# Performance work log

Hardware: AMD Instinct MI355X
Metric: run time of the kernel (lower is better)

Reference implementation:

```python
import jax, jax.numpy as jnp
import numpy as np

B, MAX_LEN, V, H, E = 256, 31, 10000, 512, 512


def setup_inputs() -> dict:
    key = jax.random.key(0)
    ks = jax.random.split(key, 10)
    s = 0.05
    return {
        "global_images": jax.random.normal(ks[0], (B, E), jnp.float32),
        "w_input": jax.random.randint(ks[1], (B, MAX_LEN), 0, V),
        "caption_lengths": jax.random.randint(ks[2], (B,), 2, MAX_LEN + 1),
        "emb": jax.random.normal(ks[3], (V, E), jnp.float32) * s,
        "W_ih": jax.random.normal(ks[4], (4 * H, 2 * E), jnp.float32) * s,
        "W_hh": jax.random.normal(ks[5], (4 * H, H), jnp.float32) * s,
        "b_ih": jax.random.normal(ks[6], (4 * H,), jnp.float32) * s,
        "b_hh": jax.random.normal(ks[7], (4 * H,), jnp.float32) * s,
        "W_out": jax.random.normal(ks[8], (V, H), jnp.float32) * s,
        "b_out": jax.random.normal(ks[9], (V,), jnp.float32) * s,
    }


def reference(global_images, w_input, caption_lengths, emb, W_ih, W_hh, b_ih, b_hh, W_out, b_out):
    # Sort by caption length, descending (mirrors torch .sort(descending=True))
    order = jnp.argsort(-caption_lengths)
    lens = caption_lengths[order]
    w = w_input[order]                      # [B, max_len]
    g = global_images[order]                # [B, E]
    target = w[:, 1:]                       # [B, max_len-1]
    dec_len = lens - 1                      # has_end_seq_token=True

    T = w.shape[1] - 1                      # max decode steps
    h0 = jnp.zeros((g.shape[0], W_hh.shape[1]), dtype=g.dtype)
    c0 = jnp.zeros_like(h0)
    words = w[:, :T].T                      # [T, B]
    ts = jnp.arange(T)

    def step(carry, inp):
        h, c = carry
        w_t, t = inp
        x_t = jnp.concatenate([g, emb[w_t]], axis=1)          # [B, 2E]
        gates = x_t @ W_ih.T + b_ih + h @ W_hh.T + b_hh       # [B, 4H]
        i, f, gg, o = jnp.split(gates, 4, axis=1)
        i, f, o = jax.nn.sigmoid(i), jax.nn.sigmoid(f), jax.nn.sigmoid(o)
        gg = jnp.tanh(gg)
        c_new = f * c + i * gg
        h_new = o * jnp.tanh(c_new)
        active = (t < dec_len)[:, None]                       # shrinking active batch
        h = jnp.where(active, h_new, h)
        c = jnp.where(active, c_new, c)
        pt = jax.nn.log_softmax(h_new @ W_out.T + b_out, axis=1)
        pt = jnp.where(active, pt, jnp.zeros((), pt.dtype))
        return (h, c), pt

    (_, _), preds = jax.lax.scan(step, (h0, c0), (words, ts))
    preds = jnp.transpose(preds, (1, 0, 2))                   # [B, T, V]
    preds = jnp.pad(preds, ((0, 0), (0, 1), (0, 0)))          # -> [B, max_len, V]
    return preds, target, dec_len
```

## Files before the change

### kernel.cpp

```cpp
#include <hip/hip_runtime.h>
#include <hip/hip_bf16.h>
#include <math.h>

#define NB   256
#define ML   31
#define NT   30
#define NV   10000
#define NH   512
#define NE   512
#define NG   2048

#define OFF_TGT  (256LL*31LL*10000LL)
#define OFF_DEC  (OFF_TGT + 256LL*30LL)
#define PRED_B   (31LL*10000LL)

typedef __attribute__((ext_vector_type(8))) short bf16x8;
typedef __attribute__((ext_vector_type(4))) float f32x4;

__device__ inline unsigned short f2bf(float f) {
    unsigned int x = __float_as_uint(f);
    unsigned int r = x + 0x7FFFu + ((x >> 16) & 1u);
    return (unsigned short)(r >> 16);
}
__device__ inline float bf2f(unsigned short u) {
    return __uint_as_float((unsigned int)u << 16);
}

__device__ inline void gl2lds16(const void* g, void* l) {
    __builtin_amdgcn_global_load_lds(
        (const __attribute__((address_space(1))) unsigned int*)g,
        (__attribute__((address_space(3))) unsigned int*)l, 16, 0, 0);
}

__global__ void sort_k(const int* __restrict__ lens, int* __restrict__ order,
                       int* __restrict__ cnt, int* __restrict__ start,
                       float* __restrict__ out_dec) {
    __shared__ int sd[NB];
    int i = threadIdx.x;
    int li = lens[i];
    int r = 0;
    for (int j = 0; j < NB; j++) {
        int lj = lens[j];
        r += (lj > li) || (lj == li && j < i);
    }
    order[r] = i;
    out_dec[r] = (float)(li - 1);
    sd[r] = li - 1;
    __syncthreads();
    if (i < NT) {
        int c = 0;
        for (int b = 0; b < NB; b++) c += (sd[b] > i);
        cnt[i] = c;
    }
    __syncthreads();
    if (i == 0) {
        int s = 0;
        for (int t = 0; t < NT; t++) { start[t] = s; s += cnt[t]; }
        start[NT] = s;
    }
}

__global__ void gather_k(const float* __restrict__ gimg, const int* __restrict__ w_in,
                         const int* __restrict__ order,
                         unsigned short* __restrict__ g_sb, int* __restrict__ wsort,
                         float* __restrict__ out_tgt) {
    int r = blockIdx.x, tid = threadIdx.x;
    int o = order[r];
    for (int e = tid; e < NE; e += 256)
        g_sb[r * NE + e] = f2bf(gimg[o * NE + e]);
    if (tid < ML) wsort[r * ML + tid] = w_in[o * ML + tid];
    if (tid < NT) out_tgt[r * NT + tid] = (float)w_in[o * ML + tid + 1];
}

__global__ void rowlist_k(const int* __restrict__ wsort, const int* __restrict__ cnt,
                          const int* __restrict__ start,
                          int* __restrict__ rowlist, int* __restrict__ rowwc) {
    int t = blockIdx.x, b = threadIdx.x;
    if (b < cnt[t]) {
        int pos = start[t] + b;
        rowlist[pos] = t * 256 + b;
        rowwc[pos] = wsort[b * ML + t];
    }
}

__global__ void f2b_k(const float* __restrict__ src, unsigned short* __restrict__ dst, int n4) {
    int i = blockIdx.x * 256 + threadIdx.x;
    if (i >= n4) return;
    float4 v = ((const float4*)src)[i];
    ushort4 o;
    o.x = f2bf(v.x); o.y = f2bf(v.y); o.z = f2bf(v.z); o.w = f2bf(v.w);
    ((ushort4*)dst)[i] = o;
}

__global__ void wih_k(const float* __restrict__ W_ih, unsigned short* __restrict__ dst, int koff) {
    int gid = blockIdx.x * 256 + threadIdx.x;
    int j = gid >> 7, k4 = gid & 127;
    float4 v = *(const float4*)(W_ih + (size_t)j * (2 * NE) + koff + k4 * 4);
    ushort4 o;
    o.x = f2bf(v.x); o.y = f2bf(v.y); o.z = f2bf(v.z); o.w = f2bf(v.w);
    *(ushort4*)(dst + (size_t)j * NE + k4 * 4) = o;
}

__global__ void wimg2_k(const float* __restrict__ W_hh, unsigned short* __restrict__ Wimg2) {
    int gid = blockIdx.x * 256 + threadIdx.x;
    int hi = gid & 3, kt = (gid >> 2) & 15, R = (gid >> 6) & 127, s = gid >> 13;
    int q = R >> 5, ct = (R >> 4) & 1, lo = R & 15;
    int col = q * 512 + s * 32 + ct * 16 + lo;
    int k = kt * 32 + hi * 8;
    const float* src = W_hh + (size_t)col * NH + k;
    __align__(16) unsigned short o[8];
#pragma unroll
    for (int j = 0; j < 8; ++j) o[j] = f2bf(src[j]);
    int ba = (R << 10) + ((kt * 64 + hi * 16) ^ ((lo & 7) << 4));
    *(uint4*)((char*)Wimg2 + ((size_t)s << 17) + ba) = *(const uint4*)o;
}

__global__ void pad_k(float* __restrict__ out) {
    int gid = blockIdx.x * 256 + threadIdx.x;
    if (gid < NB * NV) {
        int b = gid / NV, v = gid % NV;
        out[(size_t)b * PRED_B + (size_t)NT * NV + v] = 0.f;
    }
}
__global__ void zero_k(float* __restrict__ p, int n) {
    int i = blockIdx.x * 256 + threadIdx.x;
    if (i < n) p[i] = 0.f;
}

template <int AMODE, int EPI>
__launch_bounds__(256)
__global__ void bgemm(const unsigned short* __restrict__ Abf,
                      const int* __restrict__ ridx,
                      const unsigned short* __restrict__ Aemb,
                      const unsigned short* __restrict__ Bbf,
                      int N,
                      const int* __restrict__ mact_p,
                      const float* __restrict__ bias1,
                      const float* __restrict__ bias2,
                      const int* __restrict__ rowlist,
                      float* __restrict__ outf,
                      unsigned short* __restrict__ outb,
                      float* __restrict__ rowsum) {
    __shared__ __align__(16) char Bs[131072];
    int Mact = mact_p ? *mact_p : (1 << 30);
    int m0 = blockIdx.y * 128;
    if (m0 >= Mact) return;
    int n0 = blockIdx.x * 128;
    int tid = threadIdx.x;
    int lane = tid & 63, w = tid >> 6;
    int wy = w >> 1, wx = w & 1;

#pragma unroll 4
    for (int p = 0; p < 32; ++p) {
        int row = (tid >> 6) + (p << 2);
        int bn = n0 + row; if (bn > N - 1) bn = N - 1;
        uint4 v = *(const uint4*)(Bbf + ((size_t)bn << 9) + ((tid & 63) << 3));
        int ba = (row << 10) + ((tid & 63) << 4); ba ^= (row & 7) << 4;
        *(uint4*)(Bs + ba) = v;
    }

    const unsigned short* aptr[4];
#pragma unroll
    for (int rt = 0; rt < 4; ++rt) {
        int m = m0 + (wy << 6) + (rt << 4) + (lane & 15);
        if (AMODE == 0) aptr[rt] = Abf + ((size_t)m << 9);
        else {
            int mm = m < Mact ? m : (Mact - 1);
            aptr[rt] = Aemb + ((size_t)ridx[mm] << 9);
        }
    }

    f32x4 acc[4][4];
#pragma unroll
    for (int i = 0; i < 4; ++i)
#pragma unroll
        for (int j = 0; j < 4; ++j) acc[i][j] = (f32x4){0.f, 0.f, 0.f, 0.f};

    __syncthreads();

#pragma unroll 4
    for (int ks = 0; ks < 16; ++ks) {
        int koff = (ks << 5) + ((lane >> 4) << 3);
        bf16x8 bq[4];
#pragma unroll
        for (int ct = 0; ct < 4; ++ct) {
            int brow = (wx << 6) + (ct << 4) + (lane & 15);
            int bb = (brow << 10) + (koff << 1); bb ^= (brow & 7) << 4;
            bq[ct] = *(const bf16x8*)(Bs + bb);
        }
#pragma unroll
        for (int rt = 0; rt < 4; ++rt) {
            bf16x8 aq = *(const bf16x8*)(aptr[rt] + koff);
#pragma unroll
            for (int ct = 0; ct < 4; ++ct)
                acc[rt][ct] = __builtin_amdgcn_mfma_f32_16x16x32_bf16(aq, bq[ct], acc[rt][ct], 0, 0, 0);
        }
    }

#pragma unroll
    for (int rt = 0; rt < 4; ++rt) {
#pragma unroll
        for (int ct = 0; ct < 4; ++ct) {
            int n = n0 + (wx << 6) + (ct << 4) + (lane & 15);
            float badd = 0.f;
            if (EPI == 3) badd = bias1[n] + bias2[n];
#pragma unroll
            for (int ri = 0; ri < 4; ++ri) {
                int m = m0 + (wy << 6) + (rt << 4) + ((lane >> 4) << 2) + ri;
                float v = acc[rt][ct][ri] + badd;
                if (EPI == 3) {
                    outf[(size_t)m * N + n] = v;
                } else {
                    if (m < Mact) {
                        int b = rowlist[m] & 255;
                        v += bias1[(size_t)b * NG + n];
                        outb[(size_t)m * NG + ((n & 511) << 2) + (n >> 9)] = f2bf(v);
                    }
                }
            }
        }
    }
}

__launch_bounds__(256)
__global__ void ogemm(const unsigned short* __restrict__ Abf,
                      const unsigned short* __restrict__ Bbf,
                      const int* __restrict__ mact_p,
                      const float* __restrict__ bout,
                      const int* __restrict__ rowlist,
                      float* __restrict__ outf,
                      float* __restrict__ rowsum) {
    __shared__ __align__(16) char lds[65536];
    int Mact = *mact_p;
    int m0 = blockIdx.y * 128;
    if (m0 >= Mact) return;
    int n0 = blockIdx.x * 128;
    int tid = threadIdx.x;
    int lane = tid & 63, w = tid >> 6;
    int wy = w >> 1, wx = w & 1;
    int hi = lane >> 4, lo = lane & 15;

    auto stage = [&](int kt, int buf) {
#pragma unroll
        for (int i = 0; i < 4; ++i) {
            int p = (i << 8) + tid;
            int row = p >> 3, sc = (p & 7) ^ (row & 7);
            int ma = m0 + row; if (ma > Mact - 1) ma = Mact - 1;
            gl2lds16((const char*)Abf + ((size_t)ma << 10) + (kt << 7) + (sc << 4),
                     lds + (buf << 14) + (p << 4));
        }
#pragma unroll
        for (int i = 0; i < 4; ++i) {
            int p = (i << 8) + tid;
            int row = p >> 3, sc = (p & 7) ^ (row & 7);
            int nb = n0 + row; if (nb > NV - 1) nb = NV - 1;
            gl2lds16((const char*)Bbf + ((size_t)nb << 10) + (kt << 7) + (sc << 4),
                     lds + 32768 + (buf << 14) + (p << 4));
        }
    };

    f32x4 acc[4][4];
#pragma unroll
    for (int i = 0; i < 4; ++i)
#pragma unroll
        for (int j = 0; j < 4; ++j) acc[i][j] = (f32x4){0.f, 0.f, 0.f, 0.f};

    stage(0, 0);
    __syncthreads();

    for (int kt = 0; kt < 8; ++kt) {
        int buf = kt & 1;
        if (kt < 7) stage(kt + 1, buf ^ 1);
#pragma unroll
        for (int kc = 0; kc < 2; ++kc) {
            bf16x8 aq[4], bq[4];
#pragma unroll
            for (int rt = 0; rt < 4; ++rt) {
                int ra = (wy << 6) + (rt << 4) + lo;
                int cha = ((kc << 2) + hi) ^ (ra & 7);
                aq[rt] = *(const bf16x8*)(lds + (buf << 14) + (ra << 7) + (cha << 4));
                int cb = (wx << 6) + (rt << 4) + lo;
                int chb = ((kc << 2) + hi) ^ (cb & 7);
                bq[rt] = *(const bf16x8*)(lds + 32768 + (buf << 14) + (cb << 7) + (chb << 4));
            }
#pragma unroll
            for (int rt = 0; rt < 4; ++rt)
#pragma unroll
                for (int ct = 0; ct < 4; ++ct)
                    acc[rt][ct] = __builtin_amdgcn_mfma_f32_16x16x32_bf16(aq[rt], bq[ct], acc[rt][ct], 0, 0, 0);
        }
        __syncthreads();
    }

#pragma unroll
    for (int rt = 0; rt < 4; ++rt) {
        float es4[4] = {0.f, 0.f, 0.f, 0.f};
#pragma unroll
        for (int ct = 0; ct < 4; ++ct) {
            int n = n0 + (wx << 6) + (ct << 4) + lo;
            bool okn = (n < NV);
            float bo = okn ? bout[n] : 0.f;
#pragma unroll
            for (int ri = 0; ri < 4; ++ri) {
                int m = m0 + (wy << 6) + (rt << 4) + (hi << 2) + ri;
                float v = acc[rt][ct][ri] + bo;
                if (okn && m < Mact) {
                    int r = rowlist[m];
                    outf[(size_t)(r & 255) * PRED_B + (size_t)(r >> 8) * NV + n] = v;
                    es4[ri] += __expf(v);
                }
            }
        }
#pragma unroll
        for (int ri = 0; ri < 4; ++ri) {
            float s = es4[ri];
            s += __shfl_xor(s, 1); s += __shfl_xor(s, 2);
            s += __shfl_xor(s, 4); s += __shfl_xor(s, 8);
            if (lo == 0) {
                int m = m0 + (wy << 6) + (rt << 4) + (hi << 2) + ri;
                if (m < Mact) atomicAdd(&rowsum[m], s);
            }
        }
    }
}

__launch_bounds__(256, 1)
__global__ void lstmy_k(const unsigned short* __restrict__ Wimg2,
                        const unsigned short* __restrict__ gallc,
                        unsigned short* __restrict__ hx,
                        unsigned short* __restrict__ h_allc,
                        int* __restrict__ flags,
                        const int* __restrict__ cnt,
                        const int* __restrict__ start) {
    __shared__ __align__(16) char Wlds[131072];
    __shared__ __align__(16) char hlds[16384];
    __shared__ float Gs[4 * 16 * 32];
    __shared__ __align__(16) unsigned short hstg[16 * 32];
    int tid = threadIdx.x;
    int g = blockIdx.x & 15, s = blockIdx.x >> 4;
    int lane = tid & 63, w = tid >> 6;
    int hi = lane >> 4, lo = lane & 15;
    int q = w;

    {
        const char* wsrc = (const char*)Wimg2 + ((size_t)s << 17) + tid * 16;
#pragma unroll 8
        for (int r = 0; r < 32; ++r)
            gl2lds16(wsrc + r * 4096, Wlds + tid * 16 + r * 4096);
    }
    {
        uint4 z = make_uint4(0u, 0u, 0u, 0u);
        *(uint4*)(hlds + tid * 16) = z;
        *(uint4*)(hlds + 4096 + tid * 16) = z;
        *(uint4*)(hlds + 8192 + tid * 16) = z;
        *(uint4*)(hlds + 12288 + tid * 16) = z;
    }
    asm volatile("s_waitcnt vmcnt(0)" ::: "memory");
    __syncthreads();

    int row = tid >> 4, d0 = tid & 15;
    float creg[2] = {0.f, 0.f};

    for (int t = 0; t < NT; ++t) {
        int cnt_t = cnt[t];
        if (16 * g >= cnt_t) break;
        int nrow = cnt_t - 16 * g; if (nrow > 16) nrow = 16;
        int pos0 = start[t] + 16 * g;

        int rr = row < nrow ? row : nrow - 1;
        const unsigned short* gp = gallc + ((size_t)(pos0 + rr) << 11);
        uint2 gq0 = *(const uint2*)(gp + (s * 32 + d0) * 4);
        uint2 gq1 = *(const uint2*)(gp + (s * 32 + d0 + 16) * 4);

        if (t > 0) {
            if (tid < 16) {
                const int* fp = flags + g * 16 + tid;
                int f;
                do {
                    asm volatile("global_load_dword %0, %1, off sc0 sc1\n\t"
                                 "s_waitcnt vmcnt(0)"
                                 : "=v"(f) : "v"(fp) : "memory");
                } while (f < t);
            }
            __syncthreads();
            const char* hsrc = (const char*)hx +
                ((size_t)(((t - 1) & 1) * 16 + g) << 14) + tid * 16;
            uint4 va, vb, vc, vd;
            asm volatile(
                "global_load_dwordx4 %0, %4, off sc0 sc1\n\t"
                "global_load_dwordx4 %1, %5, off sc0 sc1\n\t"
                "global_load_dwordx4 %2, %6, off sc0 sc1\n\t"
                "global_load_dwordx4 %3, %7, off sc0 sc1\n\t"
                "s_waitcnt vmcnt(0)"
                : "=&v"(va), "=&v"(vb), "=&v"(vc), "=&v"(vd)
                : "v"(hsrc), "v"(hsrc + 4096), "v"(hsrc + 8192), "v"(hsrc + 12288)
                : "memory");
            *(uint4*)(hlds + tid * 16) = va;
            *(uint4*)(hlds + 4096 + tid * 16) = vb;
            *(uint4*)(hlds + 8192 + tid * 16) = vc;
            *(uint4*)(hlds + 12288 + tid * 16) = vd;
            __syncthreads();
        }

        f32x4 acc[2];
        acc[0] = (f32x4){0.f, 0.f, 0.f, 0.f};
        acc[1] = (f32x4){0.f, 0.f, 0.f, 0.f};
#pragma unroll 4
        for (int kt = 0; kt < 16; ++kt) {
            int ab = (lo << 10) + (((kt << 5) + (hi << 3)) << 1); ab ^= (lo & 7) << 4;
            bf16x8 aq = *(const bf16x8*)(hlds + ab);
#pragma unroll
            for (int ct = 0; ct < 2; ++ct) {
                int R = (q * 2 + ct) * 16 + lo;
                int bb = (R << 10) + ((kt * 64 + hi * 16) ^ ((lo & 7) << 4));
                bf16x8 bq = *(const bf16x8*)(Wlds + bb);
                acc[ct] = __builtin_amdgcn_mfma_f32_16x16x32_bf16(aq, bq, acc[ct], 0, 0, 0);
            }
        }
#pragma unroll
        for (int ct = 0; ct < 2; ++ct)
#pragma unroll
            for (int ri = 0; ri < 4; ++ri)
                Gs[(q * 16 + hi * 4 + ri) * 32 + ct * 16 + lo] = acc[ct][ri];
        __syncthreads();

        bool act = row < nrow;
#pragma unroll
        for (int p = 0; p < 2; ++p) {
            int dp = d0 + p * 16;
            int hd = s * 32 + dp;
            const unsigned short* gq = (const unsigned short*)(p ? &gq1 : &gq0);
            float iv = Gs[(0 * 16 + row) * 32 + dp] + bf2f(gq[0]);
            float fv = Gs[(1 * 16 + row) * 32 + dp] + bf2f(gq[1]);
            float gv = Gs[(2 * 16 + row) * 32 + dp] + bf2f(gq[2]);
            float ov = Gs[(3 * 16 + row) * 32 + dp] + bf2f(gq[3]);
            float i_ = 1.f / (1.f + __expf(-iv));
            float f_ = 1.f / (1.f + __expf(-fv));
            float o_ = 1.f / (1.f + __expf(-ov));
            float ea = __expf(-2.f * fabsf(gv));
            float th = (1.f - ea) / (1.f + ea);
            th = (gv < 0.f) ? -th : th;
            float cn = f_ * creg[p] + i_ * th;
            float ec = __expf(-2.f * fabsf(cn));
            float tc = (1.f - ec) / (1.f + ec);
            tc = (cn < 0.f) ? -tc : tc;
            float hn = o_ * tc;
            unsigned short hv;
            if (act) {
                creg[p] = cn;
                hv = f2bf(hn);
            } else {
                int hoff = ((row << 10) + (hd << 1)) ^ ((row & 7) << 4);
                hv = *(const unsigned short*)(hlds + hoff);
            }
            hstg[row * 32 + dp] = hv;
        }
        __syncthreads();

        if (tid < 64) {
            int crow = tid >> 2, j = tid & 3;
            uint2 v0 = *(const uint2*)(hstg + crow * 32 + j * 8);
            uint2 v1 = *(const uint2*)(hstg + crow * 32 + j * 8 + 4);
            char* himg = (char*)hx + ((size_t)((t & 1) * 16 + g) << 14);
            int dstoff = (crow << 10) + ((((s << 2) + j) ^ (crow & 7)) << 4);
            asm volatile("global_store_dwordx2 %0, %2, off sc0 sc1\n\t"
                         "global_store_dwordx2 %1, %3, off sc0 sc1"
                         :: "v"(himg + dstoff), "v"(himg + dstoff + 8),
                            "v"(v0), "v"(v1) : "memory");
            if (crow < nrow) {
                unsigned short* hap = h_allc + (size_t)(pos0 + crow) * NH + s * 32 + j * 8;
                *(uint2*)hap = v0;
                *(uint2*)(hap + 4) = v1;
            }
        }
        asm volatile("s_waitcnt vmcnt(0)" ::: "memory");
        __syncthreads();
        if (tid == 0) {
            int fv = t + 1;
            asm volatile("global_store_dword %0, %1, off sc0 sc1"
                         :: "v"(flags + g * 16 + s), "v"(fv) : "memory");
        }
    }
}

__global__ void norm_k(float* __restrict__ out, const float* __restrict__ rowsum,
                       const int* __restrict__ cnt, const int* __restrict__ start) {
    int r = blockIdx.x;
    int t = r >> 8, b = r & 255;
    bool act = b < cnt[t];
    float lse = 0.f;
    if (act) lse = logf(rowsum[start[t] + b]);
    float4* row = (float4*)(out + (size_t)b * PRED_B + (size_t)t * NV);
    for (int v4 = threadIdx.x; v4 < NV / 4; v4 += 256) {
        float4 x;
        if (act) {
            x = row[v4];
            x.x -= lse; x.y -= lse; x.z -= lse; x.w -= lse;
        } else {
            x.x = 0.f; x.y = 0.f; x.z = 0.f; x.w = 0.f;
        }
        row[v4] = x;
    }
}

extern "C" void kernel_launch(void* const* d_in, const int* in_sizes, int n_in,
                              void* d_out, int out_size, void* d_ws, size_t ws_size,
                              hipStream_t stream) {
    const float* gimg  = (const float*)d_in[0];
    const int*   w_in  = (const int*)d_in[1];
    const int*   lens  = (const int*)d_in[2];
    const float* emb   = (const float*)d_in[3];
    const float* W_ih  = (const float*)d_in[4];
    const float* W_hh  = (const float*)d_in[5];
    const float* b_ih  = (const float*)d_in[6];
    const float* b_hh  = (const float*)d_in[7];
    const float* W_out = (const float*)d_in[8];
    const float* b_out = (const float*)d_in[9];
    float* out = (float*)d_out;

    char* p = (char*)d_ws;
    auto alloc = [&](size_t bytes) -> char* {
        char* r = p;
        p += (bytes + 255) & ~(size_t)255;
        return r;
    };
    int*   order   = (int*)alloc(NB * 4);
    int*   wsort   = (int*)alloc(NB * ML * 4);
    int*   cnt     = (int*)alloc(NT * 4);
    int*   start   = (int*)alloc((NT + 1) * 4);
    int*   flags   = (int*)alloc(256 * 4);
    int*   rowlist = (int*)alloc((size_t)NT * NB * 4);
    int*   rowwc   = (int*)alloc((size_t)NT * NB * 4);
    float* gx      = (float*)alloc((size_t)NB * NG * 4);
    float* rowsum  = (float*)alloc((size_t)NT * NB * 4);
    unsigned short* g_sb   = (unsigned short*)alloc((size_t)NB * NE * 2);
    unsigned short* hx     = (unsigned short*)alloc((size_t)2 * 16 * 16384);
    unsigned short* h_allc = (unsigned short*)alloc((size_t)NT * NB * NH * 2);
    unsigned short* Wimg2  = (unsigned short*)alloc((size_t)NG * NH * 2);
    unsigned short* Wxl    = (unsigned short*)alloc((size_t)NG * NE * 2);
    unsigned short* Wxb    = (unsigned short*)alloc((size_t)NG * NE * 2);
    unsigned short* Wob    = (unsigned short*)alloc((size_t)NV * NH * 2);
    unsigned short* embb   = (unsigned short*)alloc((size_t)NV * NE * 2);
    unsigned short* gallc  = (unsigned short*)alloc((size_t)NT * NB * NG * 2);
    int* nact = start + NT;

    sort_k<<<1, 256, 0, stream>>>(lens, order, cnt, start, out + OFF_DEC);
    gather_k<<<NB, 256, 0, stream>>>(gimg, w_in, order, g_sb, wsort, out + OFF_TGT);
    rowlist_k<<<NT, 256, 0, stream>>>(wsort, cnt, start, rowlist, rowwc);
    wimg2_k<<<512, 256, 0, stream>>>(W_hh, Wimg2);
    wih_k<<<(NG * NE / 4 + 255) / 256, 256, 0, stream>>>(W_ih, Wxl, 0);
    wih_k<<<(NG * NE / 4 + 255) / 256, 256, 0, stream>>>(W_ih, Wxb, NE);
    f2b_k<<<(NV * NH / 4 + 255) / 256, 256, 0, stream>>>(W_out, Wob, NV * NH / 4);
    f2b_k<<<(NV * NE / 4 + 255) / 256, 256, 0, stream>>>(emb, embb, NV * NE / 4);
    pad_k<<<(NB * NV + 255) / 256, 256, 0, stream>>>(out);
    zero_k<<<(NT * NB + 255) / 256, 256, 0, stream>>>(rowsum, NT * NB);
    zero_k<<<1, 256, 0, stream>>>((float*)flags, 256);

    bgemm<0, 3><<<dim3(NG / 128, NB / 128), 256, 0, stream>>>(
        g_sb, nullptr, nullptr, Wxl, NG, nullptr,
        b_ih, b_hh, nullptr, gx, nullptr, nullptr);

    bgemm<1, 0><<<dim3(NG / 128, NT * NB / 128), 256, 0, stream>>>(
        nullptr, rowwc, embb, Wxb, NG, nact,
        gx, nullptr, rowlist, nullptr, gallc, nullptr);

    {
        void* cargs[] = { (void*)&Wimg2, (void*)&gallc, (void*)&hx, (void*)&h_allc,
                          (void*)&flags, (void*)&cnt, (void*)&start };
        (void)hipLaunchCooperativeKernel((void*)lstmy_k, dim3(256), dim3(256), cargs, 0, stream);
    }

    ogemm<<<dim3((NV + 127) / 128, NT * NB / 128), 256, 0, stream>>>(
        h_allc, Wob, nact, b_out, rowlist, out, rowsum);

    norm_k<<<NT * NB, 256, 0, stream>>>(out, rowsum, cnt, start);
}
```

Before: 493.5 us.

## Merge prep kernels, fold pad and zeroing, reuse pipelined GEMM for embedding gates

Merges the weight bf16 conversion kernels into one prep launch. Zeroing of flags and rowsum moves into existing kernels, and the final pad row is zeroed by norm_k. The embedding-gate GEMM now uses the double-buffered global_load_lds pipeline of the output GEMM instead of reading A directly from global memory. In the LSTM kernel, the h_allc history store is moved after the flag publish to shorten the critical path between steps. The goal is fewer launches and a faster gather GEMM, at the cost of more template complexity.

```diff
diff --git a/kernel.cpp b/kernel.cpp
--- a/kernel.cpp
+++ b/kernel.cpp
@@ -34,9 +34,10 @@
 
 __global__ void sort_k(const int* __restrict__ lens, int* __restrict__ order,
                        int* __restrict__ cnt, int* __restrict__ start,
-                       float* __restrict__ out_dec) {
+                       int* __restrict__ flags, float* __restrict__ out_dec) {
     __shared__ int sd[NB];
     int i = threadIdx.x;
+    flags[i] = 0;
     int li = lens[i];
     int r = 0;
     for (int j = 0; j < NB; j++) {
@@ -74,8 +75,10 @@
 
 __global__ void rowlist_k(const int* __restrict__ wsort, const int* __restrict__ cnt,
                           const int* __restrict__ start,
-                          int* __restrict__ rowlist, int* __restrict__ rowwc) {
+                          int* __restrict__ rowlist, int* __restrict__ rowwc,
+                          float* __restrict__ rowsum) {
     int t = blockIdx.x, b = threadIdx.x;
+    rowsum[t * 256 + b] = 0.f;
     if (b < cnt[t]) {
         int pos = start[t] + b;
         rowlist[pos] = t * 256 + b;
@@ -83,152 +86,118 @@
     }
 }
 
-__global__ void f2b_k(const float* __restrict__ src, unsigned short* __restrict__ dst, int n4) {
-    int i = blockIdx.x * 256 + threadIdx.x;
-    if (i >= n4) return;
-    float4 v = ((const float4*)src)[i];
-    ushort4 o;
-    o.x = f2bf(v.x); o.y = f2bf(v.y); o.z = f2bf(v.z); o.w = f2bf(v.w);
-    ((ushort4*)dst)[i] = o;
-}
-
-__global__ void wih_k(const float* __restrict__ W_ih, unsigned short* __restrict__ dst, int koff) {
-    int gid = blockIdx.x * 256 + threadIdx.x;
-    int j = gid >> 7, k4 = gid & 127;
-    float4 v = *(const float4*)(W_ih + (size_t)j * (2 * NE) + koff + k4 * 4);
-    ushort4 o;
-    o.x = f2bf(v.x); o.y = f2bf(v.y); o.z = f2bf(v.z); o.w = f2bf(v.w);
-    *(ushort4*)(dst + (size_t)j * NE + k4 * 4) = o;
-}
-
-__global__ void wimg2_k(const float* __restrict__ W_hh, unsigned short* __restrict__ Wimg2) {
-    int gid = blockIdx.x * 256 + threadIdx.x;
-    int hi = gid & 3, kt = (gid >> 2) & 15, R = (gid >> 6) & 127, s = gid >> 13;
-    int q = R >> 5, ct = (R >> 4) & 1, lo = R & 15;
-    int col = q * 512 + s * 32 + ct * 16 + lo;
-    int k = kt * 32 + hi * 8;
-    const float* src = W_hh + (size_t)col * NH + k;
-    __align__(16) unsigned short o[8];
-#pragma unroll
-    for (int j = 0; j < 8; ++j) o[j] = f2bf(src[j]);
-    int ba = (R << 10) + ((kt * 64 + hi * 16) ^ ((lo & 7) << 4));
-    *(uint4*)((char*)Wimg2 + ((size_t)s << 17) + ba) = *(const uint4*)o;
-}
-
-__global__ void pad_k(float* __restrict__ out) {
-    int gid = blockIdx.x * 256 + threadIdx.x;
-    if (gid < NB * NV) {
-        int b = gid / NV, v = gid % NV;
-        out[(size_t)b * PRED_B + (size_t)NT * NV + v] = 0.f;
-    }
-}
-__global__ void zero_k(float* __restrict__ p, int n) {
-    int i = blockIdx.x * 256 + threadIdx.x;
-    if (i < n) p[i] = 0.f;
+__global__ void prep_k(const float* __restrict__ W_ih, const float* __restrict__ W_hh,
+                       const float* __restrict__ W_out, const float* __restrict__ emb,
+                       unsigned short* __restrict__ Wxl, unsigned short* __restrict__ Wxb,
+                       unsigned short* __restrict__ Wob, unsigned short* __restrict__ embb,
+                       unsigned short* __restrict__ Wimg2) {
+    int bid = blockIdx.x, tid = threadIdx.x;
+    if (bid < 2048) {
+        int koff = (bid < 1024) ? 0 : NE;
+        unsigned short* dst = (bid < 1024) ? Wxl : Wxb;
+        int gid = ((bid & 1023) << 8) + tid;
+        int j = gid >> 7, k4 = gid & 127;
+        float4 v = *(const float4*)(W_ih + (size_t)j * (2 * NE) + koff + k4 * 4);
+        ushort4 o;
+        o.x = f2bf(v.x); o.y = f2bf(v.y); o.z = f2bf(v.z); o.w = f2bf(v.w);
+        *(ushort4*)(dst + (size_t)j * NE + k4 * 4) = o;
+    } else if (bid < 12048) {
+        const float* src = (bid < 7048) ? W_out : emb;
+        unsigned short* dst = (bid < 7048) ? Wob : embb;
+        int gid = ((bid < 7048 ? bid - 2048 : bid - 7048) << 8) + tid;
+        float4 v = ((const float4*)src)[gid];
+        ushort4 o;
+        o.x = f2bf(v.x); o.y = f2bf(v.y); o.z = f2bf(v.z); o.w = f2bf(v.w);
+        ((ushort4*)dst)[gid] = o;
+    } else {
+        int gid = ((bid - 12048) << 8) + tid;
+        int hi = gid & 3, kt = (gid >> 2) & 15, R = (gid >> 6) & 127, s = gid >> 13;
+        int q = R >> 5, ct = (R >> 4) & 1, lo = R & 15;
+        int col = q * 512 + s * 32 + ct * 16 + lo;
+        int k = kt * 32 + hi * 8;
+        const float* src = W_hh + (size_t)col * NH + k;
+        __align__(16) unsigned short o[8];
+#pragma unroll
+        for (int j = 0; j < 8; ++j) o[j] = f2bf(src[j]);
+        int ba = (R << 10) + ((kt * 64 + hi * 16) ^ ((lo & 7) << 4));
+        *(uint4*)((char*)Wimg2 + ((size_t)s << 17) + ba) = *(const uint4*)o;
+    }
+}
+
+__launch_bounds__(256)
+__global__ void gxgemm(const unsigned short* __restrict__ Abf,
+                       const unsigned short* __restrict__ Bbf,
+                       const float* __restrict__ bias1, const float* __restrict__ bias2,
+                       float* __restrict__ outf) {
+    __shared__ __align__(16) char Bs[131072];
+    int m0 = blockIdx.y * 128, n0 = blockIdx.x * 128;
+    int tid = threadIdx.x;
+    int lane = tid & 63, w = tid >> 6;
+    int wy = w >> 1, wx = w & 1;
+
+#pragma unroll 4
+    for (int p = 0; p < 32; ++p) {
+        int row = (tid >> 6) + (p << 2);
+        uint4 v = *(const uint4*)(Bbf + ((size_t)(n0 + row) << 9) + ((tid & 63) << 3));
+        int ba = (row << 10) + ((tid & 63) << 4); ba ^= (row & 7) << 4;
+        *(uint4*)(Bs + ba) = v;
+    }
+    const unsigned short* aptr[4];
+#pragma unroll
+    for (int rt = 0; rt < 4; ++rt)
+        aptr[rt] = Abf + ((size_t)(m0 + (wy << 6) + (rt << 4) + (lane & 15)) << 9);
+
+    f32x4 acc[4][4];
+#pragma unroll
+    for (int i = 0; i < 4; ++i)
+#pragma unroll
+        for (int j = 0; j < 4; ++j) acc[i][j] = (f32x4){0.f, 0.f, 0.f, 0.f};
+    __syncthreads();
+
+#pragma unroll 4
+    for (int ks = 0; ks < 16; ++ks) {
+        int koff = (ks << 5) + ((lane >> 4) << 3);
+        bf16x8 bq[4];
+#pragma unroll
+        for (int ct = 0; ct < 4; ++ct) {
+            int brow = (wx << 6) + (ct << 4) + (lane & 15);
+            int bb = (brow << 10) + (koff << 1); bb ^= (brow & 7) << 4;
+            bq[ct] = *(const bf16x8*)(Bs + bb);
+        }
+#pragma unroll
+        for (int rt = 0; rt < 4; ++rt) {
+            bf16x8 aq = *(const bf16x8*)(aptr[rt] + koff);
+#pragma unroll
+            for (int ct = 0; ct < 4; ++ct)
+                acc[rt][ct] = __builtin_amdgcn_mfma_f32_16x16x32_bf16(aq, bq[ct], acc[rt][ct], 0, 0, 0);
+        }
+    }
+#pragma unroll
+    for (int rt = 0; rt < 4; ++rt)
+#pragma unroll
+        for (int ct = 0; ct < 4; ++ct) {
+            int n = n0 + (wx << 6) + (ct << 4) + (lane & 15);
+            float badd = bias1[n] + bias2[n];
+#pragma unroll
+            for (int ri = 0; ri < 4; ++ri) {
+                int m = m0 + (wy << 6) + (rt << 4) + ((lane >> 4) << 2) + ri;
+                outf[(size_t)m * NG + n] = acc[rt][ct][ri] + badd;
+            }
+        }
 }
 
 template <int AMODE, int EPI>
 __launch_bounds__(256)
-__global__ void bgemm(const unsigned short* __restrict__ Abf,
+__global__ void pgemm(const unsigned short* __restrict__ Abf,
                       const int* __restrict__ ridx,
                       const unsigned short* __restrict__ Aemb,
                       const unsigned short* __restrict__ Bbf,
                       int N,
                       const int* __restrict__ mact_p,
                       const float* __restrict__ bias1,
-                      const float* __restrict__ bias2,
                       const int* __restrict__ rowlist,
                       float* __restrict__ outf,
                       unsigned short* __restrict__ outb,
-                      float* __restrict__ rowsum) {
-    __shared__ __align__(16) char Bs[131072];
-    int Mact = mact_p ? *mact_p : (1 << 30);
-    int m0 = blockIdx.y * 128;
-    if (m0 >= Mact) return;
-    int n0 = blockIdx.x * 128;
-    int tid = threadIdx.x;
-    int lane = tid & 63, w = tid >> 6;
-    int wy = w >> 1, wx = w & 1;
-
-#pragma unroll 4
-    for (int p = 0; p < 32; ++p) {
-        int row = (tid >> 6) + (p << 2);
-        int bn = n0 + row; if (bn > N - 1) bn = N - 1;
-        uint4 v = *(const uint4*)(Bbf + ((size_t)bn << 9) + ((tid & 63) << 3));
-        int ba = (row << 10) + ((tid & 63) << 4); ba ^= (row & 7) << 4;
-        *(uint4*)(Bs + ba) = v;
-    }
-
-    const unsigned short* aptr[4];
-#pragma unroll
-    for (int rt = 0; rt < 4; ++rt) {
-        int m = m0 + (wy << 6) + (rt << 4) + (lane & 15);
-        if (AMODE == 0) aptr[rt] = Abf + ((size_t)m << 9);
-        else {
-            int mm = m < Mact ? m : (Mact - 1);
-            aptr[rt] = Aemb + ((size_t)ridx[mm] << 9);
-        }
-    }
-
-    f32x4 acc[4][4];
-#pragma unroll
-    for (int i = 0; i < 4; ++i)
-#pragma unroll
-        for (int j = 0; j < 4; ++j) acc[i][j] = (f32x4){0.f, 0.f, 0.f, 0.f};
-
-    __syncthreads();
-
-#pragma unroll 4
-    for (int ks = 0; ks < 16; ++ks) {
-        int koff = (ks << 5) + ((lane >> 4) << 3);
-        bf16x8 bq[4];
-#pragma unroll
-        for (int ct = 0; ct < 4; ++ct) {
-            int brow = (wx << 6) + (ct << 4) + (lane & 15);
-            int bb = (brow << 10) + (koff << 1); bb ^= (brow & 7) << 4;
-            bq[ct] = *(const bf16x8*)(Bs + bb);
-        }
-#pragma unroll
-        for (int rt = 0; rt < 4; ++rt) {
-            bf16x8 aq = *(const bf16x8*)(aptr[rt] + koff);
-#pragma unroll
-            for (int ct = 0; ct < 4; ++ct)
-                acc[rt][ct] = __builtin_amdgcn_mfma_f32_16x16x32_bf16(aq, bq[ct], acc[rt][ct], 0, 0, 0);
-        }
-    }
-
-#pragma unroll
-    for (int rt = 0; rt < 4; ++rt) {
-#pragma unroll
-        for (int ct = 0; ct < 4; ++ct) {
-            int n = n0 + (wx << 6) + (ct << 4) + (lane & 15);
-            float badd = 0.f;
-            if (EPI == 3) badd = bias1[n] + bias2[n];
-#pragma unroll
-            for (int ri = 0; ri < 4; ++ri) {
-                int m = m0 + (wy << 6) + (rt << 4) + ((lane >> 4) << 2) + ri;
-                float v = acc[rt][ct][ri] + badd;
-                if (EPI == 3) {
-                    outf[(size_t)m * N + n] = v;
-                } else {
-                    if (m < Mact) {
-                        int b = rowlist[m] & 255;
-                        v += bias1[(size_t)b * NG + n];
-                        outb[(size_t)m * NG + ((n & 511) << 2) + (n >> 9)] = f2bf(v);
-                    }
-                }
-            }
-        }
-    }
-}
-
-__launch_bounds__(256)
-__global__ void ogemm(const unsigned short* __restrict__ Abf,
-                      const unsigned short* __restrict__ Bbf,
-                      const int* __restrict__ mact_p,
-                      const float* __restrict__ bout,
-                      const int* __restrict__ rowlist,
-                      float* __restrict__ outf,
                       float* __restrict__ rowsum) {
     __shared__ __align__(16) char lds[65536];
     int Mact = *mact_p;
@@ -240,20 +209,27 @@
     int wy = w >> 1, wx = w & 1;
     int hi = lane >> 4, lo = lane & 15;
 
+    const char* asrc[4];
+#pragma unroll
+    for (int i = 0; i < 4; ++i) {
+        int p = (i << 8) + tid;
+        int ma = m0 + (p >> 3); if (ma > Mact - 1) ma = Mact - 1;
+        if (AMODE == 0) asrc[i] = (const char*)Abf + ((size_t)ma << 10);
+        else            asrc[i] = (const char*)Aemb + ((size_t)ridx[ma] << 10);
+    }
+
     auto stage = [&](int kt, int buf) {
 #pragma unroll
         for (int i = 0; i < 4; ++i) {
             int p = (i << 8) + tid;
             int row = p >> 3, sc = (p & 7) ^ (row & 7);
-            int ma = m0 + row; if (ma > Mact - 1) ma = Mact - 1;
-            gl2lds16((const char*)Abf + ((size_t)ma << 10) + (kt << 7) + (sc << 4),
-                     lds + (buf << 14) + (p << 4));
+            gl2lds16(asrc[i] + (kt << 7) + (sc << 4), lds + (buf << 14) + (p << 4));
         }
 #pragma unroll
         for (int i = 0; i < 4; ++i) {
             int p = (i << 8) + tid;
             int row = p >> 3, sc = (p & 7) ^ (row & 7);
-            int nb = n0 + row; if (nb > NV - 1) nb = NV - 1;
+            int nb = n0 + row; if (nb > N - 1) nb = N - 1;
             gl2lds16((const char*)Bbf + ((size_t)nb << 10) + (kt << 7) + (sc << 4),
                      lds + 32768 + (buf << 14) + (p << 4));
         }
@@ -292,33 +268,51 @@
         __syncthreads();
     }
 
-#pragma unroll
-    for (int rt = 0; rt < 4; ++rt) {
-        float es4[4] = {0.f, 0.f, 0.f, 0.f};
-#pragma unroll
-        for (int ct = 0; ct < 4; ++ct) {
-            int n = n0 + (wx << 6) + (ct << 4) + lo;
-            bool okn = (n < NV);
-            float bo = okn ? bout[n] : 0.f;
+    if (EPI == 0) {
+#pragma unroll
+        for (int rt = 0; rt < 4; ++rt)
+#pragma unroll
+            for (int ct = 0; ct < 4; ++ct) {
+                int n = n0 + (wx << 6) + (ct << 4) + lo;
+#pragma unroll
+                for (int ri = 0; ri < 4; ++ri) {
+                    int m = m0 + (wy << 6) + (rt << 4) + (hi << 2) + ri;
+                    if (m < Mact) {
+                        int b = rowlist[m] & 255;
+                        float v = acc[rt][ct][ri] + bias1[(size_t)b * NG + n];
+                        outb[(size_t)m * NG + ((n & 511) << 2) + (n >> 9)] = f2bf(v);
+                    }
+                }
+            }
+    } else {
+#pragma unroll
+        for (int rt = 0; rt < 4; ++rt) {
+            float es4[4] = {0.f, 0.f, 0.f, 0.f};
+#pragma unroll
+            for (int ct = 0; ct < 4; ++ct) {
+                int n = n0 + (wx << 6) + (ct << 4) + lo;
+                bool okn = (n < N);
+                float bo = okn ? bias1[n] : 0.f;
+#pragma unroll
+                for (int ri = 0; ri < 4; ++ri) {
+                    int m = m0 + (wy << 6) + (rt << 4) + (hi << 2) + ri;
+                    float v = acc[rt][ct][ri] + bo;
+                    if (okn && m < Mact) {
+                        int r = rowlist[m];
+                        outf[(size_t)(r & 255) * PRED_B + (size_t)(r >> 8) * NV + n] = v;
+                        es4[ri] += __expf(v);
+                    }
+                }
+            }
 #pragma unroll
             for (int ri = 0; ri < 4; ++ri) {
-                int m = m0 + (wy << 6) + (rt << 4) + (hi << 2) + ri;
-                float v = acc[rt][ct][ri] + bo;
-                if (okn && m < Mact) {
-                    int r = rowlist[m];
-                    outf[(size_t)(r & 255) * PRED_B + (size_t)(r >> 8) * NV + n] = v;
-                    es4[ri] += __expf(v);
+                float s = es4[ri];
+                s += __shfl_xor(s, 1); s += __shfl_xor(s, 2);
+                s += __shfl_xor(s, 4); s += __shfl_xor(s, 8);
+                if (lo == 0) {
+                    int m = m0 + (wy << 6) + (rt << 4) + (hi << 2) + ri;
+                    if (m < Mact) atomicAdd(&rowsum[m], s);
                 }
-            }
-        }
-#pragma unroll
-        for (int ri = 0; ri < 4; ++ri) {
-            float s = es4[ri];
-            s += __shfl_xor(s, 1); s += __shfl_xor(s, 2);
-            s += __shfl_xor(s, 4); s += __shfl_xor(s, 8);
-            if (lo == 0) {
-                int m = m0 + (wy << 6) + (rt << 4) + (hi << 2) + ri;
-                if (m < Mact) atomicAdd(&rowsum[m], s);
             }
         }
     }
@@ -457,21 +451,17 @@
         }
         __syncthreads();
 
+        uint2 v0, v1;
+        int crow = tid >> 2, j = tid & 3;
         if (tid < 64) {
-            int crow = tid >> 2, j = tid & 3;
-            uint2 v0 = *(const uint2*)(hstg + crow * 32 + j * 8);
-            uint2 v1 = *(const uint2*)(hstg + crow * 32 + j * 8 + 4);
+            v0 = *(const uint2*)(hstg + crow * 32 + j * 8);
+            v1 = *(const uint2*)(hstg + crow * 32 + j * 8 + 4);
             char* himg = (char*)hx + ((size_t)((t & 1) * 16 + g) << 14);
             int dstoff = (crow << 10) + ((((s << 2) + j) ^ (crow & 7)) << 4);
             asm volatile("global_store_dwordx2 %0, %2, off sc0 sc1\n\t"
                          "global_store_dwordx2 %1, %3, off sc0 sc1"
                          :: "v"(himg + dstoff), "v"(himg + dstoff + 8),
                             "v"(v0), "v"(v1) : "memory");
-            if (crow < nrow) {
-                unsigned short* hap = h_allc + (size_t)(pos0 + crow) * NH + s * 32 + j * 8;
-                *(uint2*)hap = v0;
-                *(uint2*)(hap + 4) = v1;
-            }
         }
         asm volatile("s_waitcnt vmcnt(0)" ::: "memory");
         __syncthreads();
@@ -480,6 +470,11 @@
             asm volatile("global_store_dword %0, %1, off sc0 sc1"
                          :: "v"(flags + g * 16 + s), "v"(fv) : "memory");
         }
+        if (tid < 64 && crow < nrow) {
+            unsigned short* hap = h_allc + (size_t)(pos0 + crow) * NH + s * 32 + j * 8;
+            *(uint2*)hap = v0;
+            *(uint2*)(hap + 4) = v1;
+        }
     }
 }
 
@@ -487,7 +482,7 @@
                        const int* __restrict__ cnt, const int* __restrict__ start) {
     int r = blockIdx.x;
     int t = r >> 8, b = r & 255;
-    bool act = b < cnt[t];
+    bool act = (t < NT) && (b < cnt[t]);
     float lse = 0.f;
     if (act) lse = logf(rowsum[start[t] + b]);
     float4* row = (float4*)(out + (size_t)b * PRED_B + (size_t)t * NV);
@@ -544,25 +539,15 @@
     unsigned short* gallc  = (unsigned short*)alloc((size_t)NT * NB * NG * 2);
     int* nact = start + NT;
 
-    sort_k<<<1, 256, 0, stream>>>(lens, order, cnt, start, out + OFF_DEC);
+    sort_k<<<1, 256, 0, stream>>>(lens, order, cnt, start, flags, out + OFF_DEC);
     gather_k<<<NB, 256, 0, stream>>>(gimg, w_in, order, g_sb, wsort, out + OFF_TGT);
-    rowlist_k<<<NT, 256, 0, stream>>>(wsort, cnt, start, rowlist, rowwc);
-    wimg2_k<<<512, 256, 0, stream>>>(W_hh, Wimg2);
-    wih_k<<<(NG * NE / 4 + 255) / 256, 256, 0, stream>>>(W_ih, Wxl, 0);
-    wih_k<<<(NG * NE / 4 + 255) / 256, 256, 0, stream>>>(W_ih, Wxb, NE);
-    f2b_k<<<(NV * NH / 4 + 255) / 256, 256, 0, stream>>>(W_out, Wob, NV * NH / 4);
-    f2b_k<<<(NV * NE / 4 + 255) / 256, 256, 0, stream>>>(emb, embb, NV * NE / 4);
-    pad_k<<<(NB * NV + 255) / 256, 256, 0, stream>>>(out);
-    zero_k<<<(NT * NB + 255) / 256, 256, 0, stream>>>(rowsum, NT * NB);
-    zero_k<<<1, 256, 0, stream>>>((float*)flags, 256);
-
-    bgemm<0, 3><<<dim3(NG / 128, NB / 128), 256, 0, stream>>>(
-        g_sb, nullptr, nullptr, Wxl, NG, nullptr,
-        b_ih, b_hh, nullptr, gx, nullptr, nullptr);
-
-    bgemm<1, 0><<<dim3(NG / 128, NT * NB / 128), 256, 0, stream>>>(
-        nullptr, rowwc, embb, Wxb, NG, nact,
-        gx, nullptr, rowlist, nullptr, gallc, nullptr);
+    rowlist_k<<<NT, 256, 0, stream>>>(wsort, cnt, start, rowlist, rowwc, rowsum);
+    prep_k<<<12560, 256, 0, stream>>>(W_ih, W_hh, W_out, emb, Wxl, Wxb, Wob, embb, Wimg2);
+
+    gxgemm<<<dim3(NG / 128, NB / 128), 256, 0, stream>>>(g_sb, Wxl, b_ih, b_hh, gx);
+
+    pgemm<1, 0><<<dim3(NG / 128, NT * NB / 128), 256, 0, stream>>>(
+        nullptr, rowwc, embb, Wxb, NG, nact, gx, rowlist, nullptr, gallc, nullptr);
 
     {
         void* cargs[] = { (void*)&Wimg2, (void*)&gallc, (void*)&hx, (void*)&h_allc,
@@ -570,8 +555,8 @@
         (void)hipLaunchCooperativeKernel((void*)lstmy_k, dim3(256), dim3(256), cargs, 0, stream);
     }
 
-    ogemm<<<dim3((NV + 127) / 128, NT * NB / 128), 256, 0, stream>>>(
-        h_allc, Wob, nact, b_out, rowlist, out, rowsum);
-
-    norm_k<<<NT * NB, 256, 0, stream>>>(out, rowsum, cnt, start);
-}
+    pgemm<0, 1><<<dim3((NV + 127) / 128, NT * NB / 128), 256, 0, stream>>>(
+        h_allc, nullptr, nullptr, Wob, NV, nact, b_out, rowlist, out, nullptr, rowsum);
+
+    norm_k<<<(NT + 1) * NB, 256, 0, stream>>>(out, rowsum, cnt, start);
+}
```

Result: faster. 435.0 us (-11.8%).
